# Optimization experiments

Measured on AMD Instinct MI355X. Metric: run time of the kernel, lower is better.

The kernel has to match this reference:

```python
import jax, jax.numpy as jnp
import numpy as np

HIDDEN = 128
N_ING = 20000
N_CMP = 10000
N_EDGE = 1000000


def setup_inputs() -> dict:
    key = jax.random.key(0)
    k1, k2, k3, k4, k5, k6, k7 = jax.random.split(key, 7)
    x_ingredient = jax.random.normal(k1, (N_ING, HIDDEN), dtype=jnp.float32)
    x_compound = jax.random.normal(k2, (N_CMP, HIDDEN), dtype=jnp.float32)
    src_idx = jax.random.randint(k3, (N_EDGE,), 0, N_ING)
    dst_idx = jax.random.randint(k4, (N_EDGE,), 0, N_CMP)
    edge_index = jnp.stack([src_idx, dst_idx], axis=0)  # [2, E]
    # Linear(2H, H) then Linear(H, 1), PyTorch default init scale ~ 1/sqrt(fan_in)
    s1 = 1.0 / np.sqrt(2 * HIDDEN)
    s2 = 1.0 / np.sqrt(HIDDEN)
    W1 = jax.random.uniform(k5, (2 * HIDDEN, HIDDEN), dtype=jnp.float32, minval=-s1, maxval=s1)
    b1 = jax.random.uniform(k6, (HIDDEN,), dtype=jnp.float32, minval=-s1, maxval=s1)
    W2 = jax.random.uniform(k7, (HIDDEN, 1), dtype=jnp.float32, minval=-s2, maxval=s2)
    b2 = jnp.zeros((1,), dtype=jnp.float32)
    return {"x_ingredient": x_ingredient, "x_compound": x_compound,
            "edge_index": edge_index, "W1": W1, "b1": b1, "W2": W2, "b2": b2}


def reference(x_ingredient, x_compound, edge_index, W1, b1, W2, b2):
    src = x_ingredient[edge_index[0]]  # [E, H] gather
    dst = x_compound[edge_index[1]]    # [E, H] gather
    h = jnp.concatenate([src, dst], axis=-1)          # [E, 2H]
    h = jax.nn.relu(jnp.dot(h, W1) + b1)              # [E, H]
    out = jax.nn.sigmoid(jnp.dot(h, W2) + b2)         # [E, 1]
    return out
```

## Files before the change

### kernel.cpp

```cpp
#include <hip/hip_runtime.h>


#define H  128
#define NI 20000
#define NC 10000
#define NE 1000000

typedef _Float16 half8  __attribute__((ext_vector_type(8)));
typedef float    floatx4 __attribute__((ext_vector_type(4)));

#define P_OFF 0
#define Q_OFF (NI * H)

#define PB (NI / 16)
#define QB (NC / 16)

__launch_bounds__(256)
__global__ void pq_gemm(const float* __restrict__ xin,
                        const float* __restrict__ xcmp,
                        const float* __restrict__ W1,
                        const float* __restrict__ b1,
                        _Float16* __restrict__ ws) {
    const int b    = blockIdx.x;
    const bool isQ = (b >= PB);
    const int  rb  = (isQ ? b - PB : b) * 16;
    const float* X = isQ ? xcmp : xin;
    const int kofs = isQ ? H : 0;
    _Float16* OUT  = ws + (isQ ? Q_OFF : P_OFF);

    const int lane = threadIdx.x & 63;
    const int w    = threadIdx.x >> 6;
    const int quad = lane >> 4;
    const int m    = lane & 15;

    half8 bf[2][4];
    float b1v[2];
#pragma unroll
    for (int nt = 0; nt < 2; ++nt) {
        const int n = w * 32 + nt * 16 + m;
#pragma unroll
        for (int ks = 0; ks < 4; ++ks) {
            const int k0 = kofs + ks * 32 + quad * 8;
#pragma unroll
            for (int j = 0; j < 8; ++j)
                bf[nt][ks][j] = (_Float16)W1[(k0 + j) * H + n];
        }
        b1v[nt] = isQ ? b1[n] : 0.0f;
    }

    half8 af[4];
    const float* xr = X + (long)(rb + m) * H + quad * 8;
#pragma unroll
    for (int ks = 0; ks < 4; ++ks) {
        float4 a = *(const float4*)(xr + ks * 32);
        float4 c = *(const float4*)(xr + ks * 32 + 4);
        half8 v = { (_Float16)a.x, (_Float16)a.y, (_Float16)a.z, (_Float16)a.w,
                    (_Float16)c.x, (_Float16)c.y, (_Float16)c.z, (_Float16)c.w };
        af[ks] = v;
    }

    floatx4 acc[2] = { (floatx4)0.0f, (floatx4)0.0f };
#pragma unroll
    for (int ks = 0; ks < 4; ++ks)
#pragma unroll
        for (int nt = 0; nt < 2; ++nt)
            acc[nt] = __builtin_amdgcn_mfma_f32_16x16x32_f16(af[ks], bf[nt][ks], acc[nt], 0, 0, 0);

#pragma unroll
    for (int nt = 0; nt < 2; ++nt) {
        const int col = w * 32 + nt * 16 + m;
#pragma unroll
        for (int r = 0; r < 4; ++r) {
            const int row = rb + quad * 4 + r;
            OUT[row * H + col] = (_Float16)(acc[nt][r] + b1v[nt]);
        }
    }
}

__launch_bounds__(256)
__global__ void edge_mlp(const _Float16* __restrict__ ws,
                         const int* __restrict__ src_idx,
                         const int* __restrict__ dst_idx,
                         const float* __restrict__ W2,
                         const float* __restrict__ b2p,
                         float* __restrict__ out) {
    const int tid = threadIdx.x;
    const int c   = tid & 7;
    const int e   = blockIdx.x * 32 + (tid >> 3);

    const int s = src_idx[e];
    const int d = dst_idx[e];

    const _Float16* pr = ws + P_OFF + (long)s * H + c * 8;
    const _Float16* qr = ws + Q_OFF + (long)d * H + c * 8;

    half8 p0 = *(const half8*)(pr);
    half8 p1 = *(const half8*)(pr + 64);
    half8 q0 = *(const half8*)(qr);
    half8 q1 = *(const half8*)(qr + 64);

    const float* w2a = W2 + c * 8;
    float4 wa0 = *(const float4*)(w2a);
    float4 wa1 = *(const float4*)(w2a + 4);
    float4 wb0 = *(const float4*)(w2a + 64);
    float4 wb1 = *(const float4*)(w2a + 68);

    half8 h0 = p0 + q0;
    half8 h1 = p1 + q1;

    float acc = 0.0f;
    const float* wa = (const float*)&wa0;
    (void)wa;
#pragma unroll
    for (int i = 0; i < 4; ++i) {
        float v = fmaxf((float)h0[i], 0.0f);
        acc = fmaf(v, ((const float*)&wa0)[i], acc);
    }
#pragma unroll
    for (int i = 0; i < 4; ++i) {
        float v = fmaxf((float)h0[i + 4], 0.0f);
        acc = fmaf(v, ((const float*)&wa1)[i], acc);
    }
#pragma unroll
    for (int i = 0; i < 4; ++i) {
        float v = fmaxf((float)h1[i], 0.0f);
        acc = fmaf(v, ((const float*)&wb0)[i], acc);
    }
#pragma unroll
    for (int i = 0; i < 4; ++i) {
        float v = fmaxf((float)h1[i + 4], 0.0f);
        acc = fmaf(v, ((const float*)&wb1)[i], acc);
    }

    acc += __shfl_xor(acc, 1);
    acc += __shfl_xor(acc, 2);
    acc += __shfl_xor(acc, 4);

    if (c == 0)
        out[e] = 1.0f / (1.0f + expf(-(acc + b2p[0])));
}

extern "C" void kernel_launch(void* const* d_in, const int* in_sizes, int n_in,
                              void* d_out, int out_size, void* d_ws, size_t ws_size,
                              hipStream_t stream) {
    const float* xin  = (const float*)d_in[0];
    const float* xcmp = (const float*)d_in[1];
    const int*   eidx = (const int*)d_in[2];
    const float* W1   = (const float*)d_in[3];
    const float* b1   = (const float*)d_in[4];
    const float* W2   = (const float*)d_in[5];
    const float* b2   = (const float*)d_in[6];
    float* out = (float*)d_out;
    _Float16* ws = (_Float16*)d_ws;

    hipLaunchKernelGGL(pq_gemm, dim3(PB + QB), dim3(256), 0, stream,
                       xin, xcmp, W1, b1, ws);
    hipLaunchKernelGGL(edge_mlp, dim3(NE / 32), dim3(256), 0, stream,
                       ws, eidx, eidx + NE, W2, b2, out);
}
```

Baseline: 127.6 us.

## Quantize P/Q projection tables to int8 with global scale for edge gather

Adds a global abs-max reduction in the projection GEMM and a separate quantization kernel that converts the fp16 per-node tables to int8 with one shared scale. The edge kernel then gathers 16-byte int8 rows instead of fp16 ones and rescales the dot product before the sigmoid. This halves the random-gather traffic per edge at the cost of an extra kernel, a memset and an atomic, plus reduced precision from a single per-tensor scale.

```diff
diff --git a/kernel.cpp b/kernel.cpp
--- a/kernel.cpp
+++ b/kernel.cpp
@@ -8,9 +8,15 @@
 
 typedef _Float16 half8  __attribute__((ext_vector_type(8)));
 typedef float    floatx4 __attribute__((ext_vector_type(4)));
+typedef signed char schar16 __attribute__((ext_vector_type(16)));
+typedef signed char schar8  __attribute__((ext_vector_type(8)));
 
-#define P_OFF 0
-#define Q_OFF (NI * H)
+#define P16_OFF 0
+#define Q16_OFF (NI * H)
+#define F16_HALFS ((NI + NC) * H)
+#define P8_B   (F16_HALFS * 2)
+#define Q8_B   (P8_B + NI * H)
+#define AMAX_B (P8_B + (NI + NC) * H)
 
 #define PB (NI / 16)
 #define QB (NC / 16)
@@ -20,13 +26,13 @@
                         const float* __restrict__ xcmp,
                         const float* __restrict__ W1,
                         const float* __restrict__ b1,
-                        _Float16* __restrict__ ws) {
+                        char* __restrict__ wsb) {
     const int b    = blockIdx.x;
     const bool isQ = (b >= PB);
     const int  rb  = (isQ ? b - PB : b) * 16;
     const float* X = isQ ? xcmp : xin;
     const int kofs = isQ ? H : 0;
-    _Float16* OUT  = ws + (isQ ? Q_OFF : P_OFF);
+    _Float16* OUT  = (_Float16*)wsb + (isQ ? Q16_OFF : P16_OFF);
 
     const int lane = threadIdx.x & 63;
     const int w    = threadIdx.x >> 6;
@@ -66,19 +72,44 @@
         for (int nt = 0; nt < 2; ++nt)
             acc[nt] = __builtin_amdgcn_mfma_f32_16x16x32_f16(af[ks], bf[nt][ks], acc[nt], 0, 0, 0);
 
+    float lmax = 0.0f;
 #pragma unroll
     for (int nt = 0; nt < 2; ++nt) {
         const int col = w * 32 + nt * 16 + m;
 #pragma unroll
         for (int r = 0; r < 4; ++r) {
-            const int row = rb + quad * 4 + r;
-            OUT[row * H + col] = (_Float16)(acc[nt][r] + b1v[nt]);
+            const float v = acc[nt][r] + b1v[nt];
+            OUT[(rb + quad * 4 + r) * H + col] = (_Float16)v;
+            lmax = fmaxf(lmax, fabsf(v));
         }
+    }
+#pragma unroll
+    for (int off = 1; off < 64; off <<= 1)
+        lmax = fmaxf(lmax, __shfl_xor(lmax, off));
+    __shared__ float wred[4];
+    if (lane == 0) wred[w] = lmax;
+    __syncthreads();
+    if (threadIdx.x == 0) {
+        float bm = fmaxf(fmaxf(wred[0], wred[1]), fmaxf(wred[2], wred[3]));
+        atomicMax((unsigned*)(wsb + AMAX_B), __float_as_uint(bm));
     }
 }
 
 __launch_bounds__(256)
-__global__ void edge_mlp(const _Float16* __restrict__ ws,
+__global__ void quant(char* __restrict__ wsb) {
+    const long i = ((long)blockIdx.x * 256 + threadIdx.x) * 8;
+    const float mx  = __uint_as_float(*(const unsigned*)(wsb + AMAX_B));
+    const float inv = 127.0f / fmaxf(mx, 1e-20f);
+    half8 v = *(const half8*)((const _Float16*)wsb + i);
+    schar8 q;
+#pragma unroll
+    for (int j = 0; j < 8; ++j)
+        q[j] = (signed char)__builtin_rintf((float)v[j] * inv);
+    *(schar8*)(wsb + P8_B + i) = q;
+}
+
+__launch_bounds__(256)
+__global__ void edge_mlp(const char* __restrict__ wsb,
                          const int* __restrict__ src_idx,
                          const int* __restrict__ dst_idx,
                          const float* __restrict__ W2,
@@ -88,48 +119,43 @@
     const int c   = tid & 7;
     const int e   = blockIdx.x * 32 + (tid >> 3);
 
-    const int s = src_idx[e];
-    const int d = dst_idx[e];
+    const float mx = *(const float*)(wsb + AMAX_B);
+    const float s  = mx * (1.0f / 127.0f);
 
-    const _Float16* pr = ws + P_OFF + (long)s * H + c * 8;
-    const _Float16* qr = ws + Q_OFF + (long)d * H + c * 8;
+    const int si = src_idx[e];
+    const int di = dst_idx[e];
 
-    half8 p0 = *(const half8*)(pr);
-    half8 p1 = *(const half8*)(pr + 64);
-    half8 q0 = *(const half8*)(qr);
-    half8 q1 = *(const half8*)(qr + 64);
+    schar16 p = *(const schar16*)(wsb + P8_B + (long)si * H + c * 16);
+    schar16 q = *(const schar16*)(wsb + Q8_B + (long)di * H + c * 16);
 
-    const float* w2a = W2 + c * 8;
-    float4 wa0 = *(const float4*)(w2a);
-    float4 wa1 = *(const float4*)(w2a + 4);
-    float4 wb0 = *(const float4*)(w2a + 64);
-    float4 wb1 = *(const float4*)(w2a + 68);
-
-    half8 h0 = p0 + q0;
-    half8 h1 = p1 + q1;
+    const float* w2c = W2 + c * 16;
+    float4 wv0 = *(const float4*)(w2c);
+    float4 wv1 = *(const float4*)(w2c + 4);
+    float4 wv2 = *(const float4*)(w2c + 8);
+    float4 wv3 = *(const float4*)(w2c + 12);
+    const float* wf = (const float*)&wv0;
+    (void)wf;
 
     float acc = 0.0f;
-    const float* wa = (const float*)&wa0;
-    (void)wa;
 #pragma unroll
-    for (int i = 0; i < 4; ++i) {
-        float v = fmaxf((float)h0[i], 0.0f);
-        acc = fmaf(v, ((const float*)&wa0)[i], acc);
+    for (int j = 0; j < 4; ++j) {
+        int u = (int)p[j] + (int)q[j];
+        acc = fmaf(fmaxf((float)u, 0.0f), ((const float*)&wv0)[j], acc);
     }
 #pragma unroll
-    for (int i = 0; i < 4; ++i) {
-        float v = fmaxf((float)h0[i + 4], 0.0f);
-        acc = fmaf(v, ((const float*)&wa1)[i], acc);
+    for (int j = 0; j < 4; ++j) {
+        int u = (int)p[j + 4] + (int)q[j + 4];
+        acc = fmaf(fmaxf((float)u, 0.0f), ((const float*)&wv1)[j], acc);
     }
 #pragma unroll
-    for (int i = 0; i < 4; ++i) {
-        float v = fmaxf((float)h1[i], 0.0f);
-        acc = fmaf(v, ((const float*)&wb0)[i], acc);
+    for (int j = 0; j < 4; ++j) {
+        int u = (int)p[j + 8] + (int)q[j + 8];
+        acc = fmaf(fmaxf((float)u, 0.0f), ((const float*)&wv2)[j], acc);
     }
 #pragma unroll
-    for (int i = 0; i < 4; ++i) {
-        float v = fmaxf((float)h1[i + 4], 0.0f);
-        acc = fmaf(v, ((const float*)&wb1)[i], acc);
+    for (int j = 0; j < 4; ++j) {
+        int u = (int)p[j + 12] + (int)q[j + 12];
+        acc = fmaf(fmaxf((float)u, 0.0f), ((const float*)&wv3)[j], acc);
     }
 
     acc += __shfl_xor(acc, 1);
@@ -137,7 +163,7 @@
     acc += __shfl_xor(acc, 4);
 
     if (c == 0)
-        out[e] = 1.0f / (1.0f + expf(-(acc + b2p[0])));
+        out[e] = 1.0f / (1.0f + expf(-fmaf(s, acc, b2p[0])));
 }
 
 extern "C" void kernel_launch(void* const* d_in, const int* in_sizes, int n_in,
@@ -151,10 +177,12 @@
     const float* W2   = (const float*)d_in[5];
     const float* b2   = (const float*)d_in[6];
     float* out = (float*)d_out;
-    _Float16* ws = (_Float16*)d_ws;
+    char* wsb  = (char*)d_ws;
 
+    hipMemsetAsync(wsb + AMAX_B, 0, 4, stream);
     hipLaunchKernelGGL(pq_gemm, dim3(PB + QB), dim3(256), 0, stream,
-                       xin, xcmp, W1, b1, ws);
+                       xin, xcmp, W1, b1, wsb);
+    hipLaunchKernelGGL(quant, dim3(F16_HALFS / 8 / 256), dim3(256), 0, stream, wsb);
     hipLaunchKernelGGL(edge_mlp, dim3(NE / 32), dim3(256), 0, stream,
-                       ws, eidx, eidx + NE, W2, b2, out);
+                       wsb, eidx, eidx + NE, W2, b2, out);
 }
```

Result: slower. 151.1 us (+18.4%).

## Process five edges per thread group with index prefetch and fp16 dot2 reduction

Applied to the files above, without the earlier changes.

The edge kernel now has each block handle 160 edges in a 5-iteration loop, down from 32 edges per block. The next iteration's src/dst indices are prefetched while the current gathers are processed. W2 is converted once per thread to half2 and kept in registers, ReLU runs in packed fp16, and the dot product uses fdot2 instead of scalar fp32 FMAs. Each lane now reads 16 contiguous halves instead of two 8-half chunks 64 apart. The aim is to cut per-block overhead and ALU work in the gather-bound kernel, at the cost of some fp16 rounding in W2 and fewer blocks in flight.

```diff
diff --git a/kernel.cpp b/kernel.cpp
--- a/kernel.cpp
+++ b/kernel.cpp
@@ -6,6 +6,7 @@
 #define NC 10000
 #define NE 1000000
 
+typedef _Float16 half2v __attribute__((ext_vector_type(2)));
 typedef _Float16 half8  __attribute__((ext_vector_type(8)));
 typedef float    floatx4 __attribute__((ext_vector_type(4)));
 
@@ -70,12 +71,13 @@
     for (int nt = 0; nt < 2; ++nt) {
         const int col = w * 32 + nt * 16 + m;
 #pragma unroll
-        for (int r = 0; r < 4; ++r) {
-            const int row = rb + quad * 4 + r;
-            OUT[row * H + col] = (_Float16)(acc[nt][r] + b1v[nt]);
-        }
+        for (int r = 0; r < 4; ++r)
+            OUT[(rb + quad * 4 + r) * H + col] = (_Float16)(acc[nt][r] + b1v[nt]);
     }
 }
+
+#define EPB   160
+#define EGRID (NE / EPB)
 
 __launch_bounds__(256)
 __global__ void edge_mlp(const _Float16* __restrict__ ws,
@@ -84,60 +86,78 @@
                          const float* __restrict__ W2,
                          const float* __restrict__ b2p,
                          float* __restrict__ out) {
-    const int tid = threadIdx.x;
-    const int c   = tid & 7;
-    const int e   = blockIdx.x * 32 + (tid >> 3);
+    const int tid  = threadIdx.x;
+    const int c    = tid & 7;
+    const int slot = tid >> 3;
 
-    const int s = src_idx[e];
-    const int d = dst_idx[e];
+    half2v w2h[8];
+    const float* w2c = W2 + c * 16;
+#pragma unroll
+    for (int j = 0; j < 8; ++j) {
+        half2v t = { (_Float16)w2c[2 * j], (_Float16)w2c[2 * j + 1] };
+        w2h[j] = t;
+    }
+    const float b2v = b2p[0];
 
-    const _Float16* pr = ws + P_OFF + (long)s * H + c * 8;
-    const _Float16* qr = ws + Q_OFF + (long)d * H + c * 8;
+    int e  = blockIdx.x * EPB + slot;
+    int si = src_idx[e];
+    int di = dst_idx[e];
 
-    half8 p0 = *(const half8*)(pr);
-    half8 p1 = *(const half8*)(pr + 64);
-    half8 q0 = *(const half8*)(qr);
-    half8 q1 = *(const half8*)(qr + 64);
+#pragma unroll 1
+    for (int it = 0; it < 5; ++it) {
+        const _Float16* pr = ws + P_OFF + (long)si * H + c * 16;
+        const _Float16* qr = ws + Q_OFF + (long)di * H + c * 16;
+        half8 p0 = *(const half8*)(pr);
+        half8 p1 = *(const half8*)(pr + 8);
+        half8 q0 = *(const half8*)(qr);
+        half8 q1 = *(const half8*)(qr + 8);
 
-    const float* w2a = W2 + c * 8;
-    float4 wa0 = *(const float4*)(w2a);
-    float4 wa1 = *(const float4*)(w2a + 4);
-    float4 wb0 = *(const float4*)(w2a + 64);
-    float4 wb1 = *(const float4*)(w2a + 68);
+        int si2 = si, di2 = di;
+        if (it < 4) { si2 = src_idx[e + 32]; di2 = dst_idx[e + 32]; }
 
-    half8 h0 = p0 + q0;
-    half8 h1 = p1 + q1;
+        half8 h0 = p0 + q0;
+        half8 h1 = p1 + q1;
+        const half8 z = {};
+#if __has_builtin(__builtin_elementwise_max)
+        h0 = __builtin_elementwise_max(h0, z);
+        h1 = __builtin_elementwise_max(h1, z);
+#else
+#pragma unroll
+        for (int j = 0; j < 8; ++j) {
+            h0[j] = h0[j] > (_Float16)0 ? h0[j] : (_Float16)0;
+            h1[j] = h1[j] > (_Float16)0 ? h1[j] : (_Float16)0;
+        }
+#endif
 
-    float acc = 0.0f;
-    const float* wa = (const float*)&wa0;
-    (void)wa;
+        float acc = 0.0f;
 #pragma unroll
-    for (int i = 0; i < 4; ++i) {
-        float v = fmaxf((float)h0[i], 0.0f);
-        acc = fmaf(v, ((const float*)&wa0)[i], acc);
+        for (int j = 0; j < 4; ++j) {
+            half2v a = { h0[2 * j], h0[2 * j + 1] };
+#if __has_builtin(__builtin_amdgcn_fdot2)
+            acc = __builtin_amdgcn_fdot2(a, w2h[j], acc, false);
+#else
+            acc += (float)a[0] * (float)w2h[j][0] + (float)a[1] * (float)w2h[j][1];
+#endif
+        }
+#pragma unroll
+        for (int j = 0; j < 4; ++j) {
+            half2v a = { h1[2 * j], h1[2 * j + 1] };
+#if __has_builtin(__builtin_amdgcn_fdot2)
+            acc = __builtin_amdgcn_fdot2(a, w2h[4 + j], acc, false);
+#else
+            acc += (float)a[0] * (float)w2h[4 + j][0] + (float)a[1] * (float)w2h[4 + j][1];
+#endif
+        }
+
+        acc += __shfl_xor(acc, 1);
+        acc += __shfl_xor(acc, 2);
+        acc += __shfl_xor(acc, 4);
+
+        if (c == 0)
+            out[e] = 1.0f / (1.0f + expf(-(acc + b2v)));
+
+        e += 32; si = si2; di = di2;
     }
-#pragma unroll
-    for (int i = 0; i < 4; ++i) {
-        float v = fmaxf((float)h0[i + 4], 0.0f);
-        acc = fmaf(v, ((const float*)&wa1)[i], acc);
-    }
-#pragma unroll
-    for (int i = 0; i < 4; ++i) {
-        float v = fmaxf((float)h1[i], 0.0f);
-        acc = fmaf(v, ((const float*)&wb0)[i], acc);
-    }
-#pragma unroll
-    for (int i = 0; i < 4; ++i) {
-        float v = fmaxf((float)h1[i + 4], 0.0f);
-        acc = fmaf(v, ((const float*)&wb1)[i], acc);
-    }
-
-    acc += __shfl_xor(acc, 1);
-    acc += __shfl_xor(acc, 2);
-    acc += __shfl_xor(acc, 4);
-
-    if (c == 0)
-        out[e] = 1.0f / (1.0f + expf(-(acc + b2p[0])));
 }
 
 extern "C" void kernel_launch(void* const* d_in, const int* in_sizes, int n_in,
@@ -155,6 +175,6 @@
 
     hipLaunchKernelGGL(pq_gemm, dim3(PB + QB), dim3(256), 0, stream,
                        xin, xcmp, W1, b1, ws);
-    hipLaunchKernelGGL(edge_mlp, dim3(NE / 32), dim3(256), 0, stream,
+    hipLaunchKernelGGL(edge_mlp, dim3(EGRID), dim3(256), 0, stream,
                        ws, eidx, eidx + NE, W2, b2, out);
 }
```

After: 127.3 us. Within noise of the previous version (-0.3%).
